# Kernel optimization log

Measured on AMD Instinct MI355X. Metric: run time of the kernel, lower is better.

The kernel has to match this reference:

```python
import jax, jax.numpy as jnp
import numpy as np

NUM_HEADS = 16
ROPE_BASE = 10000.0
EPS = 1e-6


def _rms_norm(x, scale):
    # RMSNorm over last dim with learnable scale (QKNorm over full `dim`).
    var = jnp.mean(jnp.square(x), axis=-1, keepdims=True)
    return x * jax.lax.rsqrt(var + EPS) * scale


def _rotate_half(x):
    x1, x2 = jnp.split(x, 2, axis=-1)
    return jnp.concatenate([-x2, x1], axis=-1)


def _apply_rope(q, k, rotary_dim):
    # q, k: (b, n, h, d); rotate first rotary_dim channels of each head.
    n = q.shape[1]
    half = rotary_dim // 2
    inv_freq = 1.0 / (ROPE_BASE ** (jnp.arange(0, half, dtype=jnp.float32) * 2.0 / rotary_dim))
    freqs = jnp.arange(n, dtype=jnp.float32)[:, None] * inv_freq[None, :]  # (n, half)
    emb = jnp.concatenate([freqs, freqs], axis=-1)  # (n, rotary_dim)
    cos = jnp.cos(emb)[None, :, None, :]
    sin = jnp.sin(emb)[None, :, None, :]

    def rot(x):
        x_rot, x_pass = x[..., :rotary_dim], x[..., rotary_dim:]
        x_rot = x_rot * cos + _rotate_half(x_rot) * sin
        return jnp.concatenate([x_rot, x_pass], axis=-1)

    return rot(q), rot(k)


def setup_inputs() -> dict:
    key = jax.random.key(0)
    ks = jax.random.split(key, 7)
    input_dim, dim = 1024, 1024
    b, n = 2, 2048
    s_in = 1.0 / np.sqrt(input_dim)
    s_d = 1.0 / np.sqrt(dim)
    return {
        "input": jax.random.normal(ks[0], (b, n, input_dim), dtype=jnp.float32),
        "w_qkv": jax.random.normal(ks[1], (input_dim, 3 * dim), dtype=jnp.float32) * s_in,
        "b_qkv": jax.random.normal(ks[2], (3 * dim,), dtype=jnp.float32) * 0.01,
        "q_scale": jnp.ones((dim,), dtype=jnp.float32) + 0.01 * jax.random.normal(ks[3], (dim,)),
        "k_scale": jnp.ones((dim,), dtype=jnp.float32) + 0.01 * jax.random.normal(ks[4], (dim,)),
        "w_out": jax.random.normal(ks[5], (dim, input_dim), dtype=jnp.float32) * s_d,
        "b_out": jax.random.normal(ks[6], (input_dim,), dtype=jnp.float32) * 0.01,
    }


def reference(input, w_qkv, b_qkv, q_scale, k_scale, w_out, b_out):
    b, n, _ = input.shape
    h = NUM_HEADS
    qkv = input @ w_qkv + b_qkv  # (b, n, 3*dim)
    q, k, v = jnp.split(qkv, 3, axis=-1)
    q = _rms_norm(q, q_scale)
    k = _rms_norm(k, k_scale)
    d = q.shape[-1] // h
    q = q.reshape(b, n, h, d)
    k = k.reshape(b, n, h, d)
    v = v.reshape(b, n, h, d)
    q, k = _apply_rope(q, k, rotary_dim=d)  # partial_rotary_factor=1
    scale = d ** (-0.5)
    attn = jnp.einsum("bqhd,bkhd->bhqk", q, k) * scale
    attn = jax.nn.softmax(attn, axis=-1)
    out = jnp.einsum("bhqk,bkhd->bqhd", attn, v).reshape(b, n, h * d)
    return out @ w_out + b_out
```

## Files before the change

kernel.cpp:

```cpp
#include <hip/hip_runtime.h>
#include <stdint.h>

typedef short bf16x8 __attribute__((ext_vector_type(8)));
typedef float f32x4 __attribute__((ext_vector_type(4)));
typedef float f32x16 __attribute__((ext_vector_type(16)));
typedef unsigned short u16;

#define MFMA_BF16 __builtin_amdgcn_mfma_f32_16x16x32_bf16
#define MFMA32 __builtin_amdgcn_mfma_f32_32x32x16_bf16
#define LOG2E 1.44269504088896f

#if __has_builtin(__builtin_amdgcn_exp2f)
#define EXP2(x) __builtin_amdgcn_exp2f(x)
#else
#define EXP2(x) exp2f(x)
#endif

static __device__ __forceinline__ u16 f2bf(float x) {
  union { float f; unsigned u; } v; v.f = x;
  unsigned r = v.u + 0x7fffu + ((v.u >> 16) & 1u);
  return (u16)(r >> 16);
}
static __device__ __forceinline__ float bf2f(u16 h) {
  union { unsigned u; float f; } v; v.u = ((unsigned)h) << 16; return v.f;
}
static __device__ __forceinline__ unsigned cvt_pk_bf16(float lo, float hi) {
  unsigned r;
  asm("v_cvt_pk_bf16_f32 %0, %1, %2" : "=v"(r) : "v"(lo), "v"(hi));
  return r;
}
static __device__ __forceinline__ void gld_lds16(const u16* g, u16* l) {
  __builtin_amdgcn_global_load_lds(
      (const __attribute__((address_space(1))) void*)g,
      (__attribute__((address_space(3))) void*)l, 16, 0, 0);
}

__global__ __launch_bounds__(256) void k_cast(const float* __restrict__ x,
                                              u16* __restrict__ y) {
  int i = blockIdx.x * 256 + threadIdx.x;
  const float4* p = (const float4*)x;
  float4 a = p[i * 2], b = p[i * 2 + 1];
  ushort4 o0, o1;
  o0.x = f2bf(a.x); o0.y = f2bf(a.y); o0.z = f2bf(a.z); o0.w = f2bf(a.w);
  o1.x = f2bf(b.x); o1.y = f2bf(b.y); o1.z = f2bf(b.z); o1.w = f2bf(b.w);
  ushort4* q = (ushort4*)y;
  q[i * 2] = o0; q[i * 2 + 1] = o1;
}

__global__ __launch_bounds__(256) void k_wtrans(const float* __restrict__ w,
                                                u16* __restrict__ wt,
                                                int K, int N) {
  int n = blockIdx.x * 256 + threadIdx.x;
  int k0 = blockIdx.y * 8;
  if (n >= N) return;
  u16 o[8];
#pragma unroll
  for (int j = 0; j < 8; j++) o[j] = f2bf(w[(size_t)(k0 + j) * N + n]);
  *(uint4*)&wt[(size_t)n * K + k0] = *(const uint4*)o;
}

template <int OUT_BF16>
__global__ __launch_bounds__(256, 2) void k_gemm(const u16* __restrict__ A,
                                                 const u16* __restrict__ Bt,
                                                 const float* __restrict__ bias,
                                                 void* __restrict__ Cp,
                                                 int M, int N, int K) {
  __shared__ u16 As[128 * 64];
  __shared__ u16 Bs[128 * 64];
  const int tid = threadIdx.x;
  const int lane = tid & 63;
  const int wid = tid >> 6;
  const int wm = wid >> 1, wn = wid & 1;
  const int m0 = blockIdx.x * 128, n0 = blockIdx.y * 128;

  const int sr = tid >> 3;
  const int sc = tid & 7;
  const int scsw = sc ^ (sr & 7);
  const u16* ga = A + (size_t)(m0 + sr) * K + (scsw << 3);
  const u16* gb = Bt + (size_t)(n0 + sr) * K + (scsw << 3);

  const int ar = wm * 64 + (lane & 15);
  const int br = wn * 64 + (lane & 15);
  const int cs0 = lane >> 4;

  f32x4 acc[4][4] = {};

  for (int k0 = 0; k0 < K; k0 += 64) {
    __syncthreads();
#pragma unroll
    for (int i = 0; i < 4; i++)
      gld_lds16(ga + k0 + i * (32 * K), &As[((tid & ~63) + 256 * i) * 8]);
#pragma unroll
    for (int i = 0; i < 4; i++)
      gld_lds16(gb + k0 + i * (32 * K), &Bs[((tid & ~63) + 256 * i) * 8]);
    __syncthreads();
#pragma unroll
    for (int kk = 0; kk < 2; kk++) {
      bf16x8 af[4], bfr[4];
#pragma unroll
      for (int mi = 0; mi < 4; mi++)
        af[mi] = *(const bf16x8*)&As[(ar + mi * 16) * 64 +
                                     (((kk * 4 + cs0) ^ (ar & 7)) << 3)];
#pragma unroll
      for (int ni = 0; ni < 4; ni++)
        bfr[ni] = *(const bf16x8*)&Bs[(br + ni * 16) * 64 +
                                      (((kk * 4 + cs0) ^ (br & 7)) << 3)];
#pragma unroll
      for (int mi = 0; mi < 4; mi++)
#pragma unroll
        for (int ni = 0; ni < 4; ni++)
          acc[mi][ni] = MFMA_BF16(af[mi], bfr[ni], acc[mi][ni], 0, 0, 0);
    }
  }

  const int crow0 = m0 + wm * 64 + ((lane >> 4) << 2);
  const int ccol0 = n0 + wn * 64 + (lane & 15);
#pragma unroll
  for (int ni = 0; ni < 4; ni++) {
    float bv = bias[ccol0 + ni * 16];
#pragma unroll
    for (int mi = 0; mi < 4; mi++) {
#pragma unroll
      for (int r = 0; r < 4; r++) {
        float v = acc[mi][ni][r] + bv;
        size_t idx = (size_t)(crow0 + mi * 16 + r) * N + ccol0 + ni * 16;
        if (OUT_BF16) ((u16*)Cp)[idx] = f2bf(v);
        else ((float*)Cp)[idx] = v;
      }
    }
  }
}

__global__ __launch_bounds__(256) void k_normrope(const u16* __restrict__ qkv,
                                                  const float* __restrict__ qscale,
                                                  const float* __restrict__ kscale,
                                                  u16* __restrict__ Qb,
                                                  u16* __restrict__ Kb) {
  const int row = blockIdx.x;
  const int b = row >> 11, n = row & 2047;
  const int t = threadIdx.x;
  __shared__ float qn[1024], kn[1024];
  __shared__ float csb[32], snb[32];
  __shared__ float redq[4], redk[4];

  ushort4 q4 = *(const ushort4*)&qkv[(size_t)row * 3072 + t * 4];
  ushort4 k4 = *(const ushort4*)&qkv[(size_t)row * 3072 + 1024 + t * 4];
  float qv[4] = {bf2f(q4.x), bf2f(q4.y), bf2f(q4.z), bf2f(q4.w)};
  float kv[4] = {bf2f(k4.x), bf2f(k4.y), bf2f(k4.z), bf2f(k4.w)};
  float sq = 0.f, sk = 0.f;
#pragma unroll
  for (int j = 0; j < 4; j++) { sq += qv[j] * qv[j]; sk += kv[j] * kv[j]; }
#pragma unroll
  for (int o = 1; o < 64; o <<= 1) {
    sq += __shfl_xor(sq, o);
    sk += __shfl_xor(sk, o);
  }
  if ((t & 63) == 0) { redq[t >> 6] = sq; redk[t >> 6] = sk; }
  if (t < 32) {
    float inv = exp2f(-(float)t * (13.287712379549449f / 32.f));
    float fr = (float)n * inv;
    float s, c;
    sincosf(fr, &s, &c);
    csb[t] = c; snb[t] = s;
  }
  __syncthreads();
  float rq = rsqrtf((redq[0] + redq[1] + redq[2] + redq[3]) * (1.f / 1024.f) + 1e-6f);
  float rk = rsqrtf((redk[0] + redk[1] + redk[2] + redk[3]) * (1.f / 1024.f) + 1e-6f);
#pragma unroll
  for (int j = 0; j < 4; j++) {
    int jj = t * 4 + j;
    qn[jj] = qv[j] * rq * qscale[jj];
    kn[jj] = kv[j] * rk * kscale[jj];
  }
  __syncthreads();
  const int j0 = t * 4;
  const int h = j0 >> 6;
  const int d0 = j0 & 63;
  u16 qo[4], ko[4];
#pragma unroll
  for (int j = 0; j < 4; j++) {
    int jj = j0 + j;
    int dd = d0 + j;
    float c = csb[dd & 31], s = snb[dd & 31];
    float oq, ok;
    if (dd < 32) {
      oq = qn[jj] * c - qn[jj + 32] * s;
      ok = kn[jj] * c - kn[jj + 32] * s;
    } else {
      oq = qn[jj] * c + qn[jj - 32] * s;
      ok = kn[jj] * c + kn[jj - 32] * s;
    }
    qo[j] = f2bf(oq * (0.125f * LOG2E));
    ko[j] = f2bf(ok);
  }
  const size_t base = ((size_t)(b * 16 + h) * 2048 + n) * 64 + d0;
  *(ushort4*)&Qb[base] = *(const ushort4*)qo;
  *(ushort4*)&Kb[base] = *(const ushort4*)ko;
}

__global__ __launch_bounds__(256) void k_vtrans(const u16* __restrict__ qkv,
                                                u16* __restrict__ Vt) {
  const int bh = blockIdx.y;
  const int b = bh >> 4, h = bh & 15;
  const int n0 = blockIdx.x * 64;
  const int t = threadIdx.x;
  __shared__ u16 tile[64][72];
#pragma unroll
  for (int i = 0; i < 2; i++) {
    int r = (t >> 3) + 32 * i;
    int c = t & 7;
    uint4 v = *(const uint4*)&qkv[((size_t)(b * 2048 + n0 + r)) * 3072 + 2048 + h * 64 + c * 8];
    *(uint4*)&tile[r][c * 8] = v;
  }
  __syncthreads();
#pragma unroll
  for (int i = 0; i < 2; i++) {
    int dr = (t >> 3) + 32 * i;
    int c = t & 7;
    u16 vals[8];
#pragma unroll
    for (int j = 0; j < 8; j++) vals[j] = tile[c * 8 + j][dr];
    *(uint4*)&Vt[((size_t)bh * 64 + dr) * 2048 + n0 + c * 8] = *(const uint4*)vals;
  }
}

__global__ __launch_bounds__(512, 4) void k_attn(const u16* __restrict__ Qb,
                                                 const u16* __restrict__ Kb,
                                                 const u16* __restrict__ Vt,
                                                 u16* __restrict__ Ob) {
  const int bh = blockIdx.y;
  const int q0 = blockIdx.x * 128;
  const int t = threadIdx.x, lane = t & 63, wid = t >> 6;
  const int grp = wid >> 2, sub = wid & 3;
  const int q = lane & 31, hi = lane >> 5;

  __shared__ u16 smem[32768];
  u16* Ks = smem;
  u16* Vs = smem + 4 * 4096;

  const u16* Qg = Qb + (size_t)bh * 2048 * 64;
  const u16* Kg = Kb + (size_t)bh * 2048 * 64;
  const u16* Vg = Vt + (size_t)bh * 64 * 2048;

  bf16x8 qf[4];
  {
    const u16* qrow = Qg + (size_t)(q0 + sub * 32 + q) * 64;
#pragma unroll
    for (int kk = 0; kk < 4; kk++)
      qf[kk] = *(const bf16x8*)&qrow[kk * 16 + hi * 8];
  }

  f32x16 ot[2] = {};
  float lacc[4] = {0.f, 0.f, 0.f, 0.f};

  const int srow = t >> 3;
  const int sslot = (t & 7) ^ (srow & 7);
  const u16* gk = Kg + srow * 64 + (sslot << 3);
  const u16* gv = Vg + (size_t)srow * 2048 + (sslot << 3);
  const int ldoff = (t & ~63) * 8;

#define STAGE(tile)                                                     \
  do {                                                                  \
    gld_lds16(gk + (size_t)(tile) * 4096, &Ks[((tile) & 3) * 4096 + ldoff]); \
    gld_lds16(gv + (size_t)(tile) * 64,   &Vs[((tile) & 3) * 4096 + ldoff]); \
  } while (0)

  STAGE(0); STAGE(1); STAGE(2); STAGE(3);

  for (int s = 0; s < 16; ++s) {
    if (s < 15) asm volatile("s_waitcnt vmcnt(4)" ::: "memory");
    else        asm volatile("s_waitcnt vmcnt(0)" ::: "memory");
    asm volatile("s_barrier" ::: "memory");

    const int myt = 2 * s + grp;
    const u16* Kc = &Ks[(myt & 3) * 4096];
    const u16* Vc = &Vs[(myt & 3) * 4096];

    f32x16 sv0 = {}, sv1 = {};
#pragma unroll
    for (int kk = 0; kk < 4; kk++) {
      const int kr0 = 0 * 32 + q;
      const int kr1 = 1 * 32 + q;
      bf16x8 kf0 = *(const bf16x8*)&Kc[kr0 * 64 + (((kk * 2 + hi) ^ (kr0 & 7)) << 3)];
      bf16x8 kf1 = *(const bf16x8*)&Kc[kr1 * 64 + (((kk * 2 + hi) ^ (kr1 & 7)) << 3)];
      __builtin_amdgcn_s_setprio(1);
      sv0 = MFMA32(kf0, qf[kk], sv0, 0, 0, 0);
      sv1 = MFMA32(kf1, qf[kk], sv1, 0, 0, 0);
      __builtin_amdgcn_s_setprio(0);
    }

    unsigned w[2][8];
#pragma unroll
    for (int i = 0; i < 8; i++) {
      float p0 = EXP2(sv0[2 * i]);
      float p1 = EXP2(sv0[2 * i + 1]);
      lacc[i & 3] += p0 + p1;
      w[0][i] = cvt_pk_bf16(p0, p1);
    }
#pragma unroll
    for (int i = 0; i < 8; i++) {
      float p0 = EXP2(sv1[2 * i]);
      float p1 = EXP2(sv1[2 * i + 1]);
      lacc[i & 3] += p0 + p1;
      w[1][i] = cvt_pk_bf16(p0, p1);
    }

#pragma unroll
    for (int ks = 0; ks < 4; ks++) {
      const int kvt = ks >> 1, i0 = (ks & 1) * 4;
      unsigned xs0 = hi ? w[kvt][i0 + 0] : w[kvt][i0 + 2];
      unsigned xs1 = hi ? w[kvt][i0 + 1] : w[kvt][i0 + 3];
      unsigned y0 = __shfl_xor(xs0, 32);
      unsigned y1 = __shfl_xor(xs1, 32);
      union { unsigned u[4]; bf16x8 v; } pf;
      pf.u[0] = hi ? y0 : w[kvt][i0 + 0];
      pf.u[1] = hi ? y1 : w[kvt][i0 + 1];
      pf.u[2] = hi ? w[kvt][i0 + 2] : y0;
      pf.u[3] = hi ? w[kvt][i0 + 3] : y1;
#pragma unroll
      for (int dt = 0; dt < 2; dt++) {
        const int vr = dt * 32 + q;
        bf16x8 va = *(const bf16x8*)&Vc[vr * 64 + (((ks * 2 + hi) ^ (vr & 7)) << 3)];
        __builtin_amdgcn_s_setprio(1);
        ot[dt] = MFMA32(va, pf.v, ot[dt], 0, 0, 0);
        __builtin_amdgcn_s_setprio(0);
      }
    }

    asm volatile("s_barrier" ::: "memory");
    if (s < 14) { STAGE(2 * s + 4); STAGE(2 * s + 5); }
  }
#undef STAGE

  float lsum = (lacc[0] + lacc[1]) + (lacc[2] + lacc[3]);

  lsum += __shfl_xor(lsum, 32);
  __syncthreads();
  float* obuf = (float*)smem;
  float* lbuf = (float*)(smem + 16384);
  if (grp == 1) {
    float* ob = obuf + (sub * 32 + q) * 64;
#pragma unroll
    for (int dt = 0; dt < 2; dt++)
#pragma unroll
      for (int g = 0; g < 4; g++) {
        float4 v4 = {ot[dt][4 * g], ot[dt][4 * g + 1], ot[dt][4 * g + 2], ot[dt][4 * g + 3]};
        *(float4*)&ob[dt * 32 + 8 * g + 4 * hi] = v4;
      }
    if (hi == 0) lbuf[sub * 32 + q] = lsum;
  }
  __syncthreads();
  if (grp == 0) {
    const float* ob = obuf + (sub * 32 + q) * 64;
    const float invl = 1.f / (lsum + lbuf[sub * 32 + q]);
    const int b = bh >> 4, h = bh & 15;
    const int rowq = q0 + sub * 32 + q;
    u16* orow = Ob + (size_t)(b * 2048 + rowq) * 1024 + h * 64;
#pragma unroll
    for (int dt = 0; dt < 2; dt++)
#pragma unroll
      for (int g = 0; g < 4; g++) {
        float4 v4 = *(const float4*)&ob[dt * 32 + 8 * g + 4 * hi];
        u16 o4[4];
        o4[0] = f2bf((ot[dt][4 * g + 0] + v4.x) * invl);
        o4[1] = f2bf((ot[dt][4 * g + 1] + v4.y) * invl);
        o4[2] = f2bf((ot[dt][4 * g + 2] + v4.z) * invl);
        o4[3] = f2bf((ot[dt][4 * g + 3] + v4.w) * invl);
        *(ushort4*)&orow[dt * 32 + 8 * g + 4 * hi] = *(const ushort4*)o4;
      }
  }
}

extern "C" void kernel_launch(void* const* d_in, const int* in_sizes, int n_in,
                              void* d_out, int out_size, void* d_ws, size_t ws_size,
                              hipStream_t stream) {
  const float* input = (const float*)d_in[0];
  const float* w_qkv = (const float*)d_in[1];
  const float* b_qkv = (const float*)d_in[2];
  const float* q_scale = (const float*)d_in[3];
  const float* k_scale = (const float*)d_in[4];
  const float* w_out = (const float*)d_in[5];
  const float* b_out = (const float*)d_in[6];
  float* out = (float*)d_out;

  char* ws = (char*)d_ws;
  u16* Abuf  = (u16*)(ws);
  u16* WqkvT = (u16*)(ws + 8388608);
  u16* WoutT = (u16*)(ws + 14680064);
  u16* qkv   = (u16*)(ws + 16777216);
  u16* Qb    = (u16*)(ws + 41943040);
  u16* Kb    = (u16*)(ws + 50331648);
  u16* Vt    = (u16*)(ws + 58720256);
  u16* Attn  = (u16*)(ws + 67108864);

  k_cast<<<2048, 256, 0, stream>>>(input, Abuf);
  k_wtrans<<<dim3(12, 128), 256, 0, stream>>>(w_qkv, WqkvT, 1024, 3072);
  k_wtrans<<<dim3(4, 128), 256, 0, stream>>>(w_out, WoutT, 1024, 1024);
  k_gemm<1><<<dim3(32, 24), 256, 0, stream>>>(Abuf, WqkvT, b_qkv, qkv, 4096, 3072, 1024);
  k_normrope<<<4096, 256, 0, stream>>>(qkv, q_scale, k_scale, Qb, Kb);
  k_vtrans<<<dim3(32, 32), 256, 0, stream>>>(qkv, Vt);
  k_attn<<<dim3(16, 32), 512, 0, stream>>>(Qb, Kb, Vt, Attn);
  k_gemm<0><<<dim3(32, 8), 256, 0, stream>>>(Attn, WoutT, b_out, out, 4096, 1024, 1024);
}
```

Measured before the change: 131.0 us.

## Precompute RoPE table, swizzle GEMM block order, interleave QK and PV in attention

Adds a kernel that builds a cos/sin table for all positions once, so normrope loads it instead of calling sincosf in every row block. The GEMM now remaps block IDs into groups of eight to improve L2 reuse of shared tiles. In attention, the two QK^T MFMA chains are split, and the PV MFMAs for the first 32-key tile are issued before the second tile's exp, so exp work can overlap with matrix work. These add one extra launch and table traffic. The swizzle hardcodes 32 M-tiles, which holds for both GEMM launches.

Result: slower. 134.1 us (+2.3%).

```diff
diff --git a/kernel.cpp b/kernel.cpp
--- a/kernel.cpp
+++ b/kernel.cpp
@@ -57,6 +57,17 @@
 #pragma unroll
   for (int j = 0; j < 8; j++) o[j] = f2bf(w[(size_t)(k0 + j) * N + n]);
   *(uint4*)&wt[(size_t)n * K + k0] = *(const uint4*)o;
+}
+
+__global__ __launch_bounds__(256) void k_ropetab(float2* __restrict__ tab) {
+  int i = blockIdx.x * 256 + threadIdx.x;
+  int n = i >> 5, f = i & 31;
+  float inv = exp2f(-(float)f * (13.287712379549449f / 32.f));
+  float fr = (float)n * inv;
+  float s, c;
+  sincosf(fr, &s, &c);
+  float2 cs; cs.x = c; cs.y = s;
+  tab[i] = cs;
 }
 
 template <int OUT_BF16>
@@ -71,7 +82,11 @@
   const int lane = tid & 63;
   const int wid = tid >> 6;
   const int wm = wid >> 1, wn = wid & 1;
-  const int m0 = blockIdx.x * 128, n0 = blockIdx.y * 128;
+
+  const int nwg = gridDim.x * gridDim.y;
+  const int bid = blockIdx.y * gridDim.x + blockIdx.x;
+  const int swz = (bid & 7) * (nwg >> 3) + (bid >> 3);
+  const int m0 = (swz & 31) * 128, n0 = (swz >> 5) * 128;
 
   const int sr = tid >> 3;
   const int sc = tid & 7;
@@ -134,13 +149,13 @@
 __global__ __launch_bounds__(256) void k_normrope(const u16* __restrict__ qkv,
                                                   const float* __restrict__ qscale,
                                                   const float* __restrict__ kscale,
+                                                  const float2* __restrict__ tab,
                                                   u16* __restrict__ Qb,
                                                   u16* __restrict__ Kb) {
   const int row = blockIdx.x;
   const int b = row >> 11, n = row & 2047;
   const int t = threadIdx.x;
   __shared__ float qn[1024], kn[1024];
-  __shared__ float csb[32], snb[32];
   __shared__ float redq[4], redk[4];
 
   ushort4 q4 = *(const ushort4*)&qkv[(size_t)row * 3072 + t * 4];
@@ -156,12 +171,14 @@
     sk += __shfl_xor(sk, o);
   }
   if ((t & 63) == 0) { redq[t >> 6] = sq; redk[t >> 6] = sk; }
-  if (t < 32) {
-    float inv = exp2f(-(float)t * (13.287712379549449f / 32.f));
-    float fr = (float)n * inv;
-    float s, c;
-    sincosf(fr, &s, &c);
-    csb[t] = c; snb[t] = s;
+
+  const int j0 = t * 4;
+  const int d0 = j0 & 63;
+  float2 cs[4];
+  {
+    const float2* tb = tab + n * 32 + (d0 & 31);
+    *(float4*)&cs[0] = *(const float4*)&tb[0];
+    *(float4*)&cs[2] = *(const float4*)&tb[2];
   }
   __syncthreads();
   float rq = rsqrtf((redq[0] + redq[1] + redq[2] + redq[3]) * (1.f / 1024.f) + 1e-6f);
@@ -173,15 +190,13 @@
     kn[jj] = kv[j] * rk * kscale[jj];
   }
   __syncthreads();
-  const int j0 = t * 4;
   const int h = j0 >> 6;
-  const int d0 = j0 & 63;
   u16 qo[4], ko[4];
 #pragma unroll
   for (int j = 0; j < 4; j++) {
     int jj = j0 + j;
     int dd = d0 + j;
-    float c = csb[dd & 31], s = snb[dd & 31];
+    float c = cs[j].x, s = cs[j].y;
     float oq, ok;
     if (dd < 32) {
       oq = qn[jj] * c - qn[jj + 32] * s;
@@ -276,15 +291,21 @@
     const u16* Kc = &Ks[(myt & 3) * 4096];
     const u16* Vc = &Vs[(myt & 3) * 4096];
 
-    f32x16 sv0 = {}, sv1 = {};
+    f32x16 sv0 = {};
 #pragma unroll
     for (int kk = 0; kk < 4; kk++) {
-      const int kr0 = 0 * 32 + q;
-      const int kr1 = 1 * 32 + q;
+      const int kr0 = q;
       bf16x8 kf0 = *(const bf16x8*)&Kc[kr0 * 64 + (((kk * 2 + hi) ^ (kr0 & 7)) << 3)];
+      __builtin_amdgcn_s_setprio(1);
+      sv0 = MFMA32(kf0, qf[kk], sv0, 0, 0, 0);
+      __builtin_amdgcn_s_setprio(0);
+    }
+    f32x16 sv1 = {};
+#pragma unroll
+    for (int kk = 0; kk < 4; kk++) {
+      const int kr1 = 32 + q;
       bf16x8 kf1 = *(const bf16x8*)&Kc[kr1 * 64 + (((kk * 2 + hi) ^ (kr1 & 7)) << 3)];
       __builtin_amdgcn_s_setprio(1);
-      sv0 = MFMA32(kf0, qf[kk], sv0, 0, 0, 0);
       sv1 = MFMA32(kf1, qf[kk], sv1, 0, 0, 0);
       __builtin_amdgcn_s_setprio(0);
     }
@@ -298,25 +319,45 @@
       w[0][i] = cvt_pk_bf16(p0, p1);
     }
 #pragma unroll
+    for (int ks = 0; ks < 2; ks++) {
+      const int i0 = (ks & 1) * 4;
+      unsigned xs0 = hi ? w[0][i0 + 0] : w[0][i0 + 2];
+      unsigned xs1 = hi ? w[0][i0 + 1] : w[0][i0 + 3];
+      unsigned y0 = __shfl_xor(xs0, 32);
+      unsigned y1 = __shfl_xor(xs1, 32);
+      union { unsigned u[4]; bf16x8 v; } pf;
+      pf.u[0] = hi ? y0 : w[0][i0 + 0];
+      pf.u[1] = hi ? y1 : w[0][i0 + 1];
+      pf.u[2] = hi ? w[0][i0 + 2] : y0;
+      pf.u[3] = hi ? w[0][i0 + 3] : y1;
+#pragma unroll
+      for (int dt = 0; dt < 2; dt++) {
+        const int vr = dt * 32 + q;
+        bf16x8 va = *(const bf16x8*)&Vc[vr * 64 + (((ks * 2 + hi) ^ (vr & 7)) << 3)];
+        __builtin_amdgcn_s_setprio(1);
+        ot[dt] = MFMA32(va, pf.v, ot[dt], 0, 0, 0);
+        __builtin_amdgcn_s_setprio(0);
+      }
+    }
+#pragma unroll
     for (int i = 0; i < 8; i++) {
       float p0 = EXP2(sv1[2 * i]);
       float p1 = EXP2(sv1[2 * i + 1]);
       lacc[i & 3] += p0 + p1;
       w[1][i] = cvt_pk_bf16(p0, p1);
     }
-
-#pragma unroll
-    for (int ks = 0; ks < 4; ks++) {
-      const int kvt = ks >> 1, i0 = (ks & 1) * 4;
-      unsigned xs0 = hi ? w[kvt][i0 + 0] : w[kvt][i0 + 2];
-      unsigned xs1 = hi ? w[kvt][i0 + 1] : w[kvt][i0 + 3];
+#pragma unroll
+    for (int ks = 2; ks < 4; ks++) {
+      const int i0 = (ks & 1) * 4;
+      unsigned xs0 = hi ? w[1][i0 + 0] : w[1][i0 + 2];
+      unsigned xs1 = hi ? w[1][i0 + 1] : w[1][i0 + 3];
       unsigned y0 = __shfl_xor(xs0, 32);
       unsigned y1 = __shfl_xor(xs1, 32);
       union { unsigned u[4]; bf16x8 v; } pf;
-      pf.u[0] = hi ? y0 : w[kvt][i0 + 0];
-      pf.u[1] = hi ? y1 : w[kvt][i0 + 1];
-      pf.u[2] = hi ? w[kvt][i0 + 2] : y0;
-      pf.u[3] = hi ? w[kvt][i0 + 3] : y1;
+      pf.u[0] = hi ? y0 : w[1][i0 + 0];
+      pf.u[1] = hi ? y1 : w[1][i0 + 1];
+      pf.u[2] = hi ? w[1][i0 + 2] : y0;
+      pf.u[3] = hi ? w[1][i0 + 3] : y1;
 #pragma unroll
       for (int dt = 0; dt < 2; dt++) {
         const int vr = dt * 32 + q;
@@ -392,12 +433,14 @@
   u16* Kb    = (u16*)(ws + 50331648);
   u16* Vt    = (u16*)(ws + 58720256);
   u16* Attn  = (u16*)(ws + 67108864);
+  float2* Rt = (float2*)(ws + 75497472);
 
   k_cast<<<2048, 256, 0, stream>>>(input, Abuf);
   k_wtrans<<<dim3(12, 128), 256, 0, stream>>>(w_qkv, WqkvT, 1024, 3072);
   k_wtrans<<<dim3(4, 128), 256, 0, stream>>>(w_out, WoutT, 1024, 1024);
+  k_ropetab<<<256, 256, 0, stream>>>(Rt);
   k_gemm<1><<<dim3(32, 24), 256, 0, stream>>>(Abuf, WqkvT, b_qkv, qkv, 4096, 3072, 1024);
-  k_normrope<<<4096, 256, 0, stream>>>(qkv, q_scale, k_scale, Qb, Kb);
+  k_normrope<<<4096, 256, 0, stream>>>(qkv, q_scale, k_scale, Rt, Qb, Kb);
   k_vtrans<<<dim3(32, 32), 256, 0, stream>>>(qkv, Vt);
   k_attn<<<dim3(16, 32), 512, 0, stream>>>(Qb, Kb, Vt, Attn);
   k_gemm<0><<<dim3(32, 8), 256, 0, stream>>>(Attn, WoutT, b_out, out, 4096, 1024, 1024);
```
